# Performance work log

Measured on AMD Instinct MI355X. Metric: run time of the kernel, lower is better.

The kernel has to match this reference:

```python
import jax, jax.numpy as jnp
import numpy as np

C, K, D_LLM = 32, 16, 768
B, L, D_MODEL = 8, 512, 256
H, D_KEYS = 8, 32
TEMP = 1.0 / np.sqrt(D_KEYS)


def setup_inputs() -> dict:
    key = jax.random.key(0)
    ks = jax.random.split(key, 8)
    topk = jax.random.normal(ks[0], (C, K, D_LLM), dtype=jnp.float32)
    ts_emb = jax.random.normal(ks[1], (B, L, D_MODEL), dtype=jnp.float32)
    probs = jax.random.uniform(ks[2], (B, L, C), dtype=jnp.float32)
    probs = probs / jnp.sum(probs, axis=-1, keepdims=True)  # soft cluster probabilities
    scale = 0.02  # keep pre-softmax logits in a stable range
    q_proj = jax.random.normal(ks[3], (C, H * D_KEYS, D_MODEL + 1), dtype=jnp.float32) * scale
    k_proj = jax.random.normal(ks[4], (C, H * D_KEYS, D_LLM + 1), dtype=jnp.float32) * scale
    v_proj = jax.random.normal(ks[5], (C, H * D_KEYS, D_LLM + 1), dtype=jnp.float32) * scale
    out_w = jax.random.normal(ks[6], (C, H, D_KEYS, D_LLM), dtype=jnp.float32) * scale
    out_b = jax.random.normal(ks[7], (C, D_LLM), dtype=jnp.float32) * scale
    return {"topk_token_embeddings": topk, "ts_emb": ts_emb, "cluster_probs": probs,
            "q_proj": q_proj, "k_proj": k_proj, "v_proj": v_proj,
            "out_w": out_w, "out_b": out_b}


def reference(topk_token_embeddings, ts_emb, cluster_probs, q_proj, k_proj, v_proj, out_w, out_b):
    b, l, _ = ts_emb.shape
    c, k, d_llm = topk_token_embeddings.shape
    # per-cluster Q/K/V projections (weights have an extra trailing bias column)
    q = jnp.einsum('bld,cgd->blcg', ts_emb, q_proj[..., :-1]) + q_proj[..., -1]
    q = q.reshape(b, l, c, H, D_KEYS)
    kk = jnp.einsum('ckd,cgd->kcg', topk_token_embeddings, k_proj[..., :-1]) + k_proj[..., -1]
    kk = kk.reshape(k, c, H, D_KEYS)
    v = jnp.einsum('ckd,cgd->kcg', topk_token_embeddings, v_proj[..., :-1]) + v_proj[..., -1]
    v = v.reshape(k, c, H, D_KEYS)
    # cross attention over the k retrieved tokens, per cluster and head
    att = jnp.einsum('blchd,kchd->bchlk', q, kk)  # (B,c,H,L,k)
    att = jax.nn.softmax(TEMP * att, axis=-1)  # dropout disabled (eval)
    out_v = jnp.einsum('bchlk,kchd->bclhd', att, v)
    aligned = jnp.einsum('bclhd,chde->blce', out_v, out_w) + out_b  # (B,L,c,d_llm)
    fused = jnp.sum(aligned * cluster_probs[:, :, :, None], axis=-2)  # (B,L,d_llm)
    return fused
```

## Files before the change

### kernel.cpp

```cpp
#include <hip/hip_runtime.h>
#include <hip/hip_bf16.h>

#define C_   32
#define K_   16
#define DLLM 768
#define DM   256
#define H_   8
#define DK   32
#define G_   256
#define BL   4096
#define NN   4096
#define E_   768
#define LDP  4160
#define TEMPF 0.17677669529663687f
#define SCL2  0.2550348647f

typedef __attribute__((ext_vector_type(8))) short bf16x8;
typedef __attribute__((ext_vector_type(4))) float f32x4;
typedef unsigned int u32;

__device__ __forceinline__ unsigned short f2bf(float f) {
    unsigned int u = __float_as_uint(f);
    unsigned int r = (u + 0x7fffu + ((u >> 16) & 1u)) >> 16;
    return (unsigned short)r;
}
__device__ __forceinline__ float bf2f(unsigned int u) {
    return __uint_as_float(u << 16);
}

__device__ __forceinline__ void gl16(const void* g, void* l) {
    __builtin_amdgcn_global_load_lds(
        (const __attribute__((address_space(1))) u32*)g,
        (__attribute__((address_space(3))) u32*)l, 16, 0, 0);
}

__global__ __launch_bounds__(256) void k1_kv(const float* __restrict__ topk,
                                             const float* __restrict__ kp,
                                             const float* __restrict__ vp,
                                             float* __restrict__ kk,
                                             float* __restrict__ vv) {
    const int c  = blockIdx.x;
    const int gq = blockIdx.y;
    const int t = threadIdx.x;
    const int lane = t & 63, w = t >> 6;

    __shared__ float t_l[K_][DLLM];
    {
        const float4* src = reinterpret_cast<const float4*>(topk + (size_t)c * K_ * DLLM);
        float4* dst = reinterpret_cast<float4*>(&t_l[0][0]);
#pragma unroll
        for (int i = 0; i < 12; ++i)
            dst[t + i * 256] = src[t + i * 256];
    }
    __syncthreads();

#pragma unroll
    for (int gi = 0; gi < 4; ++gi) {
        const int g = gq * 16 + w * 4 + gi;
        const float* kpr = kp + (size_t)(c * G_ + g) * (DLLM + 1);
        const float* vpr = vp + (size_t)(c * G_ + g) * (DLLM + 1);
        const float bk = kpr[DLLM], bv = vpr[DLLM];
        float acck[K_] = {}, accv[K_] = {};
#pragma unroll
        for (int r = 0; r < 3; ++r) {
            const int d = r * 256 + lane * 4;
            float4 wk = *reinterpret_cast<const float4*>(kpr + d);
            float4 wv = *reinterpret_cast<const float4*>(vpr + d);
#pragma unroll
            for (int k = 0; k < K_; ++k) {
                float4 t4 = *reinterpret_cast<const float4*>(&t_l[k][d]);
                acck[k] += wk.x * t4.x + wk.y * t4.y + wk.z * t4.z + wk.w * t4.w;
                accv[k] += wv.x * t4.x + wv.y * t4.y + wv.z * t4.z + wv.w * t4.w;
            }
        }
#pragma unroll
        for (int s = 32; s >= 1; s >>= 1) {
#pragma unroll
            for (int k = 0; k < K_; ++k) {
                acck[k] += __shfl_xor(acck[k], s);
                accv[k] += __shfl_xor(accv[k], s);
            }
        }
        if (lane == 0) {
#pragma unroll
            for (int k = 0; k < K_; ++k) {
                kk[(size_t)(c * K_ + k) * G_ + g] = acck[k] + bk;
                vv[(size_t)(c * K_ + k) * G_ + g] = accv[k] + bv;
            }
        }
    }
}

__global__ __launch_bounds__(256) void k0_cvt(const float* __restrict__ ts,
                                              const float* __restrict__ probs,
                                              const float* __restrict__ outb,
                                              unsigned short* __restrict__ tsb,
                                              unsigned short* __restrict__ P,
                                              unsigned short* __restrict__ VWt) {
    const int bid = blockIdx.x, t = threadIdx.x;
    if (bid < 1024) {
        const int idx = bid * 1024 + t * 4;
        float4 v = *reinterpret_cast<const float4*>(ts + idx);
        uint2 o;
        o.x = f2bf(v.x) | ((unsigned)f2bf(v.y) << 16);
        o.y = f2bf(v.z) | ((unsigned)f2bf(v.w) << 16);
        *reinterpret_cast<uint2*>(tsb + idx) = o;
    } else if (bid < 1056) {
        const int b2 = bid - 1024;
        const int row = b2 * 128 + (t >> 1);
        const int ch = (t & 1) * 16;
        unsigned short o[16];
#pragma unroll
        for (int j = 0; j < 16; ++j) o[j] = f2bf(probs[row * 32 + ch + j]);
        uint4 u0, u1;
        u0.x = o[0] | (o[1] << 16);  u0.y = o[2] | (o[3] << 16);
        u0.z = o[4] | (o[5] << 16);  u0.w = o[6] | (o[7] << 16);
        u1.x = o[8] | (o[9] << 16);  u1.y = o[10] | (o[11] << 16);
        u1.z = o[12] | (o[13] << 16); u1.w = o[14] | (o[15] << 16);
        unsigned short* dst = P + (size_t)row * LDP + 4096 + ch;
        *reinterpret_cast<uint4*>(dst) = u0;
        *reinterpret_cast<uint4*>(dst + 8) = u1;
        uint4 z = {0u, 0u, 0u, 0u};
        unsigned short* pz = P + (size_t)row * LDP + 4128 + ch;
        *reinterpret_cast<uint4*>(pz) = z;
        *reinterpret_cast<uint4*>(pz + 8) = z;
    } else {
        const int idx = (bid - 1056) * 256 + t;
        const int e = idx >> 5, cc = idx & 31;
        VWt[(size_t)e * LDP + 4096 + cc] = f2bf(outb[cc * E_ + e]);
        VWt[(size_t)e * LDP + 4128 + cc] = 0;
    }
}

__global__ __launch_bounds__(768) void k23(const float* __restrict__ qp,
                                           const float* __restrict__ kk,
                                           const float* __restrict__ ow,
                                           const float* __restrict__ vv,
                                           unsigned short* __restrict__ A2t,
                                           float* __restrict__ abias,
                                           unsigned short* __restrict__ VWt) {
    const int c = blockIdx.x, h = blockIdx.y;
    const int t = threadIdx.x;
    __shared__ float kk_l[K_][DK];
    __shared__ float v_l[K_][DK];
    __shared__ float bq_l[DK];
    if (t < 512) {
        int k = t / DK, d = t % DK;
        kk_l[k][d] = kk[(size_t)(c * K_ + k) * G_ + h * DK + d];
        v_l[k][d]  = vv[(size_t)(c * K_ + k) * G_ + h * DK + d];
    }
    if (t < DK)
        bq_l[t] = qp[(size_t)(c * G_ + h * DK + t) * (DM + 1) + DM];
    __syncthreads();
    const int ch = c * H_ + h;
    {
        const int e = t;
        float acc[K_];
#pragma unroll
        for (int k = 0; k < K_; ++k) acc[k] = 0.f;
        for (int d = 0; d < DK; ++d) {
            float w = ow[((size_t)ch * DK + d) * E_ + e];
#pragma unroll
            for (int k = 0; k < K_; ++k) acc[k] += w * v_l[k][d];
        }
#pragma unroll
        for (int k = 0; k < K_; ++k)
            VWt[(size_t)e * LDP + ch * 16 + k] = f2bf(acc[k]);
    }
    if (t < 256) {
        const int m = t;
        float acc[K_];
#pragma unroll
        for (int k = 0; k < K_; ++k) acc[k] = 0.f;
        for (int d = 0; d < DK; ++d) {
            float wq = qp[(size_t)(c * G_ + h * DK + d) * (DM + 1) + m];
#pragma unroll
            for (int k = 0; k < K_; ++k) acc[k] += wq * kk_l[k][d];
        }
#pragma unroll
        for (int k = 0; k < K_; ++k)
            A2t[(size_t)(ch * 16 + k) * DM + m] = f2bf(acc[k] * SCL2);
        if (m < K_) {
            float s = 0.f;
#pragma unroll
            for (int d = 0; d < DK; ++d) s += bq_l[d] * kk_l[m][d];
            abias[ch * 16 + m] = s * SCL2;
        }
    }
}

__global__ __launch_bounds__(256, 2) void k4_att(const unsigned short* __restrict__ A2t,
                                                 const unsigned short* __restrict__ tsb,
                                                 const float* __restrict__ abias,
                                                 const float* __restrict__ probs,
                                                 unsigned short* __restrict__ P) {
    const int n0  = blockIdx.x * 128;
    const int bl0 = blockIdx.y * 256;
    const int t = threadIdx.x;
    const int lane = t & 63, w = t >> 6;
    const int wr = w >> 1, wc = w & 1;
    const int c = lane & 15, g = lane >> 4;
    const int rsl = (c >> 1) & 3;

    __shared__ unsigned short a_l[2][128 * 32];
    __shared__ unsigned short b_l[2][256 * 32];
    __shared__ float ab_l[128];
    __shared__ float pb_l[256];

    if (t < 128) ab_l[t] = abias[n0 + t];
    pb_l[t] = probs[(size_t)(bl0 + t) * C_ + (n0 >> 7)];

    const int srow = t >> 2;
    const int sw = ((t & 3) ^ ((t >> 3) & 3)) * 8;

    f32x4 acc[4][8] = {};

#pragma unroll
    for (int j = 0; j < 2; ++j)
        gl16(A2t + (size_t)(n0 + j * 64 + srow) * DM + sw, &a_l[0][j * 2048 + t * 8]);
#pragma unroll
    for (int j = 0; j < 4; ++j)
        gl16(tsb + (size_t)(bl0 + j * 64 + srow) * DM + sw, &b_l[0][j * 2048 + t * 8]);
    __syncthreads();

    for (int kt = 0; kt < 8; ++kt) {
        const int cur = kt & 1;
        if (kt < 7) {
            const int col = (kt + 1) * 32 + sw;
#pragma unroll
            for (int j = 0; j < 2; ++j)
                gl16(A2t + (size_t)(n0 + j * 64 + srow) * DM + col,
                     &a_l[cur ^ 1][j * 2048 + t * 8]);
#pragma unroll
            for (int j = 0; j < 4; ++j)
                gl16(tsb + (size_t)(bl0 + j * 64 + srow) * DM + col,
                     &b_l[cur ^ 1][j * 2048 + t * 8]);
        }
        bf16x8 af[4], bfr[8];
#pragma unroll
        for (int a = 0; a < 4; ++a)
            af[a] = *reinterpret_cast<const bf16x8*>(
                &a_l[cur][(wr * 64 + a * 16 + c) * 32 + (g ^ rsl) * 8]);
#pragma unroll
        for (int b = 0; b < 8; ++b)
            bfr[b] = *reinterpret_cast<const bf16x8*>(
                &b_l[cur][(wc * 128 + b * 16 + c) * 32 + (g ^ rsl) * 8]);
#pragma unroll
        for (int a = 0; a < 4; ++a)
#pragma unroll
            for (int b = 0; b < 8; ++b)
                acc[a][b] = __builtin_amdgcn_mfma_f32_16x16x32_bf16(af[a], bfr[b], acc[a][b], 0, 0, 0);
        __syncthreads();
    }

#pragma unroll
    for (int a = 0; a < 4; ++a) {
        const int nbase = wr * 64 + a * 16 + g * 4;
#pragma unroll
        for (int b = 0; b < 8; ++b) {
            const int bll = wc * 128 + b * 16 + c;
            float e0 = __builtin_amdgcn_exp2f(acc[a][b][0] + ab_l[nbase + 0]);
            float e1 = __builtin_amdgcn_exp2f(acc[a][b][1] + ab_l[nbase + 1]);
            float e2 = __builtin_amdgcn_exp2f(acc[a][b][2] + ab_l[nbase + 2]);
            float e3 = __builtin_amdgcn_exp2f(acc[a][b][3] + ab_l[nbase + 3]);
            float s = (e0 + e1) + (e2 + e3);
            s += __shfl_xor(s, 16);
            s += __shfl_xor(s, 32);
            const float pv = pb_l[bll] * __builtin_amdgcn_rcpf(s);
            unsigned r0, r1;
            float p0 = e0 * pv, p1 = e1 * pv, p2 = e2 * pv, p3 = e3 * pv;
            asm("v_cvt_pk_bf16_f32 %0, %1, %2" : "=v"(r0) : "v"(p0), "v"(p1));
            asm("v_cvt_pk_bf16_f32 %0, %1, %2" : "=v"(r1) : "v"(p2), "v"(p3));
            uint2 o; o.x = r0; o.y = r1;
            *reinterpret_cast<uint2*>(P + (size_t)(bl0 + bll) * LDP + n0 + nbase) = o;
        }
    }
}

__global__ __launch_bounds__(256, 2) void k5_out(const unsigned short* __restrict__ P,
                                                 const unsigned short* __restrict__ VWt,
                                                 unsigned short* __restrict__ part) {
    const int wg = blockIdx.x;
    const int xcd = wg & 7;
    const int local = wg >> 3;
    const int bl0 = (xcd * 4 + (local & 3)) * 128;
    const int e0  = ((local >> 2) & 3) * 192;
    const int ks  = local >> 4;

    const int t = threadIdx.x;
    const int lane = t & 63, w = t >> 6;
    const int wr = w >> 1, wc = w & 1;
    const int c = lane & 15, g = lane >> 4;
    const int rsl = (c >> 1) & 3;

    __shared__ unsigned short a_l[2][128 * 32];
    __shared__ unsigned short b_l[2][192 * 32];

    const int nstart = ks * 1024;
    const int nsteps = (ks == 3) ? 34 : 32;

    const int srow = t >> 2;
    const int sw = ((t & 3) ^ ((t >> 3) & 3)) * 8;

#pragma unroll
    for (int j = 0; j < 2; ++j)
        gl16(P + (size_t)(bl0 + j * 64 + srow) * LDP + nstart + sw,
             &a_l[0][j * 2048 + t * 8]);
#pragma unroll
    for (int j = 0; j < 3; ++j)
        gl16(VWt + (size_t)(e0 + j * 64 + srow) * LDP + nstart + sw,
             &b_l[0][j * 2048 + t * 8]);
    __syncthreads();

    f32x4 acc[4][6] = {};
    for (int kt = 0; kt < nsteps; ++kt) {
        const int cur = kt & 1;
        if (kt + 1 < nsteps) {
            const int col = nstart + (kt + 1) * 32 + sw;
#pragma unroll
            for (int j = 0; j < 2; ++j)
                gl16(P + (size_t)(bl0 + j * 64 + srow) * LDP + col,
                     &a_l[cur ^ 1][j * 2048 + t * 8]);
#pragma unroll
            for (int j = 0; j < 3; ++j)
                gl16(VWt + (size_t)(e0 + j * 64 + srow) * LDP + col,
                     &b_l[cur ^ 1][j * 2048 + t * 8]);
        }
        bf16x8 af[4], bfr[6];
#pragma unroll
        for (int a = 0; a < 4; ++a)
            af[a] = *reinterpret_cast<const bf16x8*>(
                &a_l[cur][(wr * 64 + a * 16 + c) * 32 + (g ^ rsl) * 8]);
#pragma unroll
        for (int b = 0; b < 6; ++b)
            bfr[b] = *reinterpret_cast<const bf16x8*>(
                &b_l[cur][(wc * 96 + b * 16 + c) * 32 + (g ^ rsl) * 8]);
#pragma unroll
        for (int a = 0; a < 4; ++a)
#pragma unroll
            for (int b = 0; b < 6; ++b)
                acc[a][b] = __builtin_amdgcn_mfma_f32_16x16x32_bf16(af[a], bfr[b], acc[a][b], 0, 0, 0);
        __syncthreads();
    }

    unsigned short* pp = part + ((size_t)ks * BL + bl0) * E_ + e0;
#pragma unroll
    for (int a = 0; a < 4; ++a)
#pragma unroll
        for (int b = 0; b < 6; ++b)
#pragma unroll
            for (int i = 0; i < 4; ++i)
                pp[(size_t)(wr * 64 + a * 16 + g * 4 + i) * E_ + wc * 96 + b * 16 + c] =
                    f2bf(acc[a][b][i]);
}

__global__ __launch_bounds__(256) void k6_red(const unsigned short* __restrict__ part,
                                              float* __restrict__ out) {
    const size_t base = ((size_t)blockIdx.x * 256 + threadIdx.x) * 8;
    float s[8] = {};
#pragma unroll
    for (int ks = 0; ks < 4; ++ks) {
        uint4 v = *reinterpret_cast<const uint4*>(part + (size_t)ks * (BL * E_) + base);
        const unsigned u[4] = {v.x, v.y, v.z, v.w};
#pragma unroll
        for (int j = 0; j < 4; ++j) {
            s[2 * j]     += bf2f(u[j] & 0xffffu);
            s[2 * j + 1] += bf2f(u[j] >> 16);
        }
    }
    *reinterpret_cast<float4*>(out + base)     = make_float4(s[0], s[1], s[2], s[3]);
    *reinterpret_cast<float4*>(out + base + 4) = make_float4(s[4], s[5], s[6], s[7]);
}

extern "C" void kernel_launch(void* const* d_in, const int* in_sizes, int n_in,
                              void* d_out, int out_size, void* d_ws, size_t ws_size,
                              hipStream_t stream) {
    const float* topk  = (const float*)d_in[0];
    const float* ts    = (const float*)d_in[1];
    const float* probs = (const float*)d_in[2];
    const float* qp    = (const float*)d_in[3];
    const float* kp    = (const float*)d_in[4];
    const float* vp    = (const float*)d_in[5];
    const float* ow    = (const float*)d_in[6];
    const float* ob    = (const float*)d_in[7];
    float* out = (float*)d_out;

    char* wp = (char*)d_ws;
    float* kk            = (float*)wp;           wp += 524288;
    float* vv            = (float*)wp;           wp += 524288;
    float* ab            = (float*)wp;           wp += 16384;
    unsigned short* tsb  = (unsigned short*)wp;  wp += 2097152;
    unsigned short* A2t  = (unsigned short*)wp;  wp += 2097152;
    unsigned short* VWt  = (unsigned short*)wp;  wp += (size_t)E_ * LDP * 2;
    unsigned short* P    = (unsigned short*)wp;  wp += (size_t)BL * LDP * 2;
    unsigned short* part = (unsigned short*)wp;

    k1_kv <<<dim3(32, 16), 256, 0, stream>>>(topk, kp, vp, kk, vv);
    k0_cvt<<<1152,         256, 0, stream>>>(ts, probs, ob, tsb, P, VWt);
    k23   <<<dim3(32, 8),  768, 0, stream>>>(qp, kk, ow, vv, A2t, ab, VWt);
    k4_att<<<dim3(32, 16), 256, 0, stream>>>(A2t, tsb, ab, probs, P);
    k5_out<<<512,          256, 0, stream>>>(P, VWt, part);
    k6_red<<<1536,         256, 0, stream>>>(part, out);
}
```

Baseline: 115.3 us.

## Triple-buffer LDS staging with explicit vmcnt waits in attention and output GEMMs

Both the k4 attention GEMM and the k5 output GEMM move from double to triple buffering of their shared-memory tiles. Each now keeps two global-to-LDS loads in flight and replaces __syncthreads with explicit s_waitcnt vmcnt counts plus raw s_barrier. The goal is to hide more global memory latency behind the MFMA work. The cost is more LDS per block, which may cut occupancy at 2 blocks per CU. The hand-counted vmcnt values assume the compiler emits exactly that many vector memory ops per stage, so a wrong count could cause races.

```diff
diff --git a/kernel.cpp b/kernel.cpp
--- a/kernel.cpp
+++ b/kernel.cpp
@@ -202,8 +202,8 @@
     const int c = lane & 15, g = lane >> 4;
     const int rsl = (c >> 1) & 3;
 
-    __shared__ unsigned short a_l[2][128 * 32];
-    __shared__ unsigned short b_l[2][256 * 32];
+    __shared__ unsigned short a_l[3][128 * 32];
+    __shared__ unsigned short b_l[3][256 * 32];
     __shared__ float ab_l[128];
     __shared__ float pb_l[256];
 
@@ -213,45 +213,55 @@
     const int srow = t >> 2;
     const int sw = ((t & 3) ^ ((t >> 3) & 3)) * 8;
 
+#define K4_STAGE(buf, kt)                                                         \
+    {                                                                             \
+        const int col_ = (kt) * 32 + sw;                                          \
+        _Pragma("unroll")                                                         \
+        for (int j = 0; j < 2; ++j)                                               \
+            gl16(A2t + (size_t)(n0 + j * 64 + srow) * DM + col_,                  \
+                 &a_l[buf][j * 2048 + t * 8]);                                    \
+        _Pragma("unroll")                                                         \
+        for (int j = 0; j < 4; ++j)                                               \
+            gl16(tsb + (size_t)(bl0 + j * 64 + srow) * DM + col_,                 \
+                 &b_l[buf][j * 2048 + t * 8]);                                    \
+    }
+
+    K4_STAGE(0, 0)
+    K4_STAGE(1, 1)
+    asm volatile("s_waitcnt lgkmcnt(0)" ::: "memory");
+
     f32x4 acc[4][8] = {};
 
 #pragma unroll
-    for (int j = 0; j < 2; ++j)
-        gl16(A2t + (size_t)(n0 + j * 64 + srow) * DM + sw, &a_l[0][j * 2048 + t * 8]);
-#pragma unroll
-    for (int j = 0; j < 4; ++j)
-        gl16(tsb + (size_t)(bl0 + j * 64 + srow) * DM + sw, &b_l[0][j * 2048 + t * 8]);
-    __syncthreads();
-
     for (int kt = 0; kt < 8; ++kt) {
-        const int cur = kt & 1;
-        if (kt < 7) {
-            const int col = (kt + 1) * 32 + sw;
-#pragma unroll
-            for (int j = 0; j < 2; ++j)
-                gl16(A2t + (size_t)(n0 + j * 64 + srow) * DM + col,
-                     &a_l[cur ^ 1][j * 2048 + t * 8]);
-#pragma unroll
-            for (int j = 0; j < 4; ++j)
-                gl16(tsb + (size_t)(bl0 + j * 64 + srow) * DM + col,
-                     &b_l[cur ^ 1][j * 2048 + t * 8]);
-        }
+        const int bcur = kt % 3;
+        if (kt < 6) {
+            K4_STAGE((kt + 2) % 3, kt + 2)
+            asm volatile("s_waitcnt vmcnt(12)" ::: "memory");
+        } else if (kt == 6) {
+            asm volatile("s_waitcnt vmcnt(6)" ::: "memory");
+        } else {
+            asm volatile("s_waitcnt vmcnt(0)" ::: "memory");
+        }
+        asm volatile("s_barrier" ::: "memory");
         bf16x8 af[4], bfr[8];
 #pragma unroll
         for (int a = 0; a < 4; ++a)
             af[a] = *reinterpret_cast<const bf16x8*>(
-                &a_l[cur][(wr * 64 + a * 16 + c) * 32 + (g ^ rsl) * 8]);
+                &a_l[bcur][(wr * 64 + a * 16 + c) * 32 + (g ^ rsl) * 8]);
 #pragma unroll
         for (int b = 0; b < 8; ++b)
             bfr[b] = *reinterpret_cast<const bf16x8*>(
-                &b_l[cur][(wc * 128 + b * 16 + c) * 32 + (g ^ rsl) * 8]);
+                &b_l[bcur][(wc * 128 + b * 16 + c) * 32 + (g ^ rsl) * 8]);
 #pragma unroll
         for (int a = 0; a < 4; ++a)
 #pragma unroll
             for (int b = 0; b < 8; ++b)
                 acc[a][b] = __builtin_amdgcn_mfma_f32_16x16x32_bf16(af[a], bfr[b], acc[a][b], 0, 0, 0);
-        __syncthreads();
-    }
+        if (kt < 7)
+            asm volatile("s_barrier" ::: "memory");
+    }
+#undef K4_STAGE
 
 #pragma unroll
     for (int a = 0; a < 4; ++a) {
@@ -293,8 +303,8 @@
     const int c = lane & 15, g = lane >> 4;
     const int rsl = (c >> 1) & 3;
 
-    __shared__ unsigned short a_l[2][128 * 32];
-    __shared__ unsigned short b_l[2][192 * 32];
+    __shared__ unsigned short a_l[3][128 * 32];
+    __shared__ unsigned short b_l[3][192 * 32];
 
     const int nstart = ks * 1024;
     const int nsteps = (ks == 3) ? 34 : 32;
@@ -302,46 +312,52 @@
     const int srow = t >> 2;
     const int sw = ((t & 3) ^ ((t >> 3) & 3)) * 8;
 
-#pragma unroll
-    for (int j = 0; j < 2; ++j)
-        gl16(P + (size_t)(bl0 + j * 64 + srow) * LDP + nstart + sw,
-             &a_l[0][j * 2048 + t * 8]);
-#pragma unroll
-    for (int j = 0; j < 3; ++j)
-        gl16(VWt + (size_t)(e0 + j * 64 + srow) * LDP + nstart + sw,
-             &b_l[0][j * 2048 + t * 8]);
-    __syncthreads();
+#define K5_STAGE(buf, kt)                                                         \
+    {                                                                             \
+        const int col_ = nstart + (kt) * 32 + sw;                                 \
+        _Pragma("unroll")                                                         \
+        for (int j = 0; j < 2; ++j)                                               \
+            gl16(P + (size_t)(bl0 + j * 64 + srow) * LDP + col_,                  \
+                 &a_l[buf][j * 2048 + t * 8]);                                    \
+        _Pragma("unroll")                                                         \
+        for (int j = 0; j < 3; ++j)                                               \
+            gl16(VWt + (size_t)(e0 + j * 64 + srow) * LDP + col_,                 \
+                 &b_l[buf][j * 2048 + t * 8]);                                    \
+    }
+
+    K5_STAGE(0, 0)
+    K5_STAGE(1, 1)
 
     f32x4 acc[4][6] = {};
     for (int kt = 0; kt < nsteps; ++kt) {
-        const int cur = kt & 1;
-        if (kt + 1 < nsteps) {
-            const int col = nstart + (kt + 1) * 32 + sw;
-#pragma unroll
-            for (int j = 0; j < 2; ++j)
-                gl16(P + (size_t)(bl0 + j * 64 + srow) * LDP + col,
-                     &a_l[cur ^ 1][j * 2048 + t * 8]);
-#pragma unroll
-            for (int j = 0; j < 3; ++j)
-                gl16(VWt + (size_t)(e0 + j * 64 + srow) * LDP + col,
-                     &b_l[cur ^ 1][j * 2048 + t * 8]);
-        }
+        const int bcur = kt % 3;
+        if (kt + 2 < nsteps) {
+            K5_STAGE((kt + 2) % 3, kt + 2)
+            asm volatile("s_waitcnt vmcnt(10)" ::: "memory");
+        } else if (kt + 1 < nsteps) {
+            asm volatile("s_waitcnt vmcnt(5)" ::: "memory");
+        } else {
+            asm volatile("s_waitcnt vmcnt(0)" ::: "memory");
+        }
+        asm volatile("s_barrier" ::: "memory");
         bf16x8 af[4], bfr[6];
 #pragma unroll
         for (int a = 0; a < 4; ++a)
             af[a] = *reinterpret_cast<const bf16x8*>(
-                &a_l[cur][(wr * 64 + a * 16 + c) * 32 + (g ^ rsl) * 8]);
+                &a_l[bcur][(wr * 64 + a * 16 + c) * 32 + (g ^ rsl) * 8]);
 #pragma unroll
         for (int b = 0; b < 6; ++b)
             bfr[b] = *reinterpret_cast<const bf16x8*>(
-                &b_l[cur][(wc * 96 + b * 16 + c) * 32 + (g ^ rsl) * 8]);
+                &b_l[bcur][(wc * 96 + b * 16 + c) * 32 + (g ^ rsl) * 8]);
 #pragma unroll
         for (int a = 0; a < 4; ++a)
 #pragma unroll
             for (int b = 0; b < 6; ++b)
                 acc[a][b] = __builtin_amdgcn_mfma_f32_16x16x32_bf16(af[a], bfr[b], acc[a][b], 0, 0, 0);
-        __syncthreads();
-    }
+        if (kt + 1 < nsteps)
+            asm volatile("s_barrier" ::: "memory");
+    }
+#undef K5_STAGE
 
     unsigned short* pp = part + ((size_t)ks * BL + bl0) * E_ + e0;
 #pragma unroll
```

Result: no change. 113.4 us (-1.7%).
